# Kernel optimization log

Hardware: AMD Instinct MI355X
Metric: run time of the kernel (lower is better)

## Reference

```python
import jax, jax.numpy as jnp
import numpy as np

C = 512
NH = 4
HD = C // NH
G = 32  # min(32, C) and C % 32 == 0
EPS = 1e-5


def setup_inputs() -> dict:
    key = jax.random.key(0)
    ks = jax.random.split(key, 11)
    s = 1.0 / np.sqrt(C)
    return {
        "x": jax.random.normal(ks[0], (16, C, 32, 32), dtype=jnp.float32),
        "gamma": jnp.ones((C,), jnp.float32),
        "beta": jnp.zeros((C,), jnp.float32),
        "wq": jax.random.normal(ks[1], (C, C), jnp.float32) * s,
        "bq": jax.random.normal(ks[2], (C,), jnp.float32) * 0.01,
        "wk": jax.random.normal(ks[3], (C, C), jnp.float32) * s,
        "bk": jax.random.normal(ks[4], (C,), jnp.float32) * 0.01,
        "wv": jax.random.normal(ks[5], (C, C), jnp.float32) * s,
        "bv": jax.random.normal(ks[6], (C,), jnp.float32) * 0.01,
        "wp": jax.random.normal(ks[7], (C, C), jnp.float32) * s,
        "bp": jax.random.normal(ks[8], (C,), jnp.float32) * 0.01,
    }


def _group_norm(x, gamma, beta):
    b, c, h, w = x.shape
    xr = x.reshape(b, G, c // G, h, w)
    mean = xr.mean(axis=(2, 3, 4), keepdims=True)
    var = xr.var(axis=(2, 3, 4), keepdims=True)
    xn = ((xr - mean) * jax.lax.rsqrt(var + EPS)).reshape(b, c, h, w)
    return xn * gamma[None, :, None, None] + beta[None, :, None, None]


def _conv1x1(x, w, b):
    # 1x1 conv == per-position channel GEMM
    return jnp.einsum('oc,bchw->bohw', w, x) + b[None, :, None, None]


def reference(x, gamma, beta, wq, bq, wk, bk, wv, bv, wp, bp):
    b, c, h, w = x.shape
    hw = h * w
    scale = HD ** (-0.5)
    hn = _group_norm(x, gamma, beta)
    q = _conv1x1(hn, wq, bq).reshape(b, NH, HD, hw)
    k = _conv1x1(hn, wk, bk).reshape(b, NH, HD, hw)
    v = _conv1x1(hn, wv, bv).reshape(b, NH, HD, hw)
    attn = jnp.einsum('bhdq,bhdk->bhqk', q, k) * scale  # [b, nh, hw, hw]
    attn = jax.nn.softmax(attn, axis=-1)
    out = jnp.einsum('bhqk,bhdk->bhdq', attn, v)  # [b, nh, hd, hw]
    out = out.reshape(b, c, h, w)
    out = _conv1x1(out, wp, bp)
    return x + out
```

## Files before the change

### kernel.cpp

```cpp
#include <hip/hip_runtime.h>
#include <math.h>

#define CCH 512
#define NH 4
#define HD 128
#define HW 1024
#define BATCH 16
#define EPS 1e-5f

typedef __attribute__((ext_vector_type(8))) short bfrag;
typedef __attribute__((ext_vector_type(4))) float f4;
typedef __attribute__((ext_vector_type(16))) float f16v;

static __device__ __forceinline__ unsigned short f2bf(float f) {
  union { float f; unsigned u; } v;
  v.f = f;
  unsigned r = v.u + 0x7fff + ((v.u >> 16) & 1);
  return (unsigned short)(r >> 16);
}
static __device__ __forceinline__ unsigned cvt_pk_bf16(float a, float b) {
  unsigned r;
  asm("v_cvt_pk_bf16_f32 %0, %1, %2" : "=v"(r) : "v"(a), "v"(b));
  return r;
}
#if defined(__has_builtin) && __has_builtin(__builtin_amdgcn_exp2f)
#define EXP2(x) __builtin_amdgcn_exp2f(x)
#else
#define EXP2(x) __expf((x) * 0.6931471805599453f)
#endif
static __device__ __forceinline__ void ldg_lds16(const unsigned short* g,
                                                 unsigned short* l) {
  __builtin_amdgcn_global_load_lds(
      (const __attribute__((address_space(1))) unsigned int*)g,
      (__attribute__((address_space(3))) unsigned int*)l, 16, 0, 0);
}

#define QSCALE (0.08838834764831845f * 1.4426950408889634f)

#define SWZ(r) (((r) ^ ((r) >> 2)) & 3)

__global__ __launch_bounds__(256) void gnw_kernel(
    const float* __restrict__ x, const float* __restrict__ gamma,
    const float* __restrict__ beta, unsigned short* __restrict__ hn,
    const float* __restrict__ wq, const float* __restrict__ wk,
    const float* __restrict__ wv, const float* __restrict__ wp,
    unsigned short* __restrict__ wB) {
  int bx = blockIdx.x;
  int t = threadIdx.x;
  if (bx >= 512) {
    int i0 = bx - 512;
    int mat = i0 >> 8;
    const float* srcs[4] = {wq, wk, wv, wp};
    const float* s = srcs[mat];
    unsigned short* dp = wB + (size_t)mat * CCH * CCH;
    int i = (i0 & 255) * 256 + t;
    f4 v = ((const f4*)s)[i];
    uint2 o;
    o.x = cvt_pk_bf16(v.x, v.y);
    o.y = cvt_pk_bf16(v.z, v.w);
    *(uint2*)&((ushort4*)dp)[i] = o;
    return;
  }
  int b = bx >> 5, g = bx & 31;
  const float* xp = x + ((size_t)b * CCH + g * 16) * HW;
  float s = 0.f, ss = 0.f;
  const f4* xp4 = (const f4*)xp;
  f4 vv[16];
#pragma unroll
  for (int c = 0; c < 16; ++c) {
    f4 v = xp4[c * 256 + t];
    vv[c] = v;
    s += v.x + v.y + v.z + v.w;
    ss += v.x * v.x + v.y * v.y + v.z * v.z + v.w * v.w;
  }
#pragma unroll
  for (int off = 32; off > 0; off >>= 1) {
    s += __shfl_xor(s, off);
    ss += __shfl_xor(ss, off);
  }
  __shared__ float rs[4], rss[4];
  int w = t >> 6;
  if ((t & 63) == 0) { rs[w] = s; rss[w] = ss; }
  __syncthreads();
  s = rs[0] + rs[1] + rs[2] + rs[3];
  ss = rss[0] + rss[1] + rss[2] + rss[3];
  const float invn = 1.f / (16 * HW);
  float mean = s * invn;
  float var = ss * invn - mean * mean;
  float rstd = rsqrtf(var + EPS);
  float a_[16], b_[16];
#pragma unroll
  for (int c = 0; c < 16; ++c) {
    float gm = gamma[g * 16 + c] * rstd;
    a_[c] = gm;
    b_[c] = beta[g * 16 + c] - mean * gm;
  }
#pragma unroll
  for (int i = 0; i < 4; ++i) {
    int p = 4 * t + i;
    uint4 u0, u1;
    u0.x = cvt_pk_bf16(vv[0][i] * a_[0] + b_[0], vv[1][i] * a_[1] + b_[1]);
    u0.y = cvt_pk_bf16(vv[2][i] * a_[2] + b_[2], vv[3][i] * a_[3] + b_[3]);
    u0.z = cvt_pk_bf16(vv[4][i] * a_[4] + b_[4], vv[5][i] * a_[5] + b_[5]);
    u0.w = cvt_pk_bf16(vv[6][i] * a_[6] + b_[6], vv[7][i] * a_[7] + b_[7]);
    u1.x = cvt_pk_bf16(vv[8][i] * a_[8] + b_[8], vv[9][i] * a_[9] + b_[9]);
    u1.y = cvt_pk_bf16(vv[10][i] * a_[10] + b_[10], vv[11][i] * a_[11] + b_[11]);
    u1.z = cvt_pk_bf16(vv[12][i] * a_[12] + b_[12], vv[13][i] * a_[13] + b_[13]);
    u1.w = cvt_pk_bf16(vv[14][i] * a_[14] + b_[14], vv[15][i] * a_[15] + b_[15]);
    unsigned short* dst = hn + ((size_t)b * HW + p) * CCH + g * 16;
    *(uint4*)dst = u0;
    *(uint4*)(dst + 8) = u1;
  }
}

template <int MODE>
__global__ __launch_bounds__(256, 3) void mm_kernel(
    const unsigned short* __restrict__ Xt, const unsigned short* __restrict__ Wb,
    const float* __restrict__ b0, const float* __restrict__ b1,
    const float* __restrict__ resid,
    unsigned short* __restrict__ O0, unsigned short* __restrict__ O1,
    float* __restrict__ Ofp) {
  int b = blockIdx.z;
  int p0 = blockIdx.x * 128;
  int c0g = blockIdx.y * 128;
  __shared__ __align__(16) unsigned short S_[24576];
  int t = threadIdx.x;
  int w = t >> 6, lane = t & 63, l15 = lane & 15, quad = lane >> 4;
  int wp = (w & 1) * 64, wc = (w >> 1) * 64;
  const unsigned short* Xb = Xt + (size_t)b * HW * CCH;
  const unsigned short* Wr = Wb + (size_t)c0g * CCH;
  f4 acc[4][4] = {};
  auto stage = [&](int k0, int bi) {
    unsigned short* Xd = S_ + bi * 8192;
    unsigned short* Wd = Xd + 4096;
#pragma unroll
    for (int j = 0; j < 2; ++j) {
      int chk = w * 2 + j;
      int r = chk * 16 + (lane >> 2);
      int c = (lane & 3) ^ SWZ(r);
      ldg_lds16(&Xb[(size_t)(p0 + r) * CCH + k0 + c * 8], Xd + chk * 512);
      ldg_lds16(&Wr[(size_t)r * CCH + k0 + c * 8], Wd + chk * 512);
    }
  };
  stage(0, 0);
  stage(32, 1);
  int cur = 0;
  for (int k0 = 0; k0 < CCH; k0 += 32) {
    if (k0 < CCH - 32)
      asm volatile("s_waitcnt vmcnt(4)" ::: "memory");
    else
      asm volatile("s_waitcnt vmcnt(0)" ::: "memory");
    __builtin_amdgcn_s_barrier();
    __builtin_amdgcn_sched_barrier(0);
    if (k0 + 64 < CCH) stage(k0 + 64, cur ? cur - 1 : 2);
    const unsigned short* Xc = S_ + cur * 8192;
    const unsigned short* Wc = Xc + 4096;
    bfrag af[4], bf[4];
#pragma unroll
    for (int pt = 0; pt < 4; ++pt) {
      int r = wp + pt * 16 + l15;
      af[pt] = *(const bfrag*)&Xc[r * 32 + ((quad ^ SWZ(r)) << 3)];
    }
#pragma unroll
    for (int ct = 0; ct < 4; ++ct) {
      int r = wc + ct * 16 + l15;
      bf[ct] = *(const bfrag*)&Wc[r * 32 + ((quad ^ SWZ(r)) << 3)];
    }
#pragma unroll
    for (int pt = 0; pt < 4; ++pt)
#pragma unroll
      for (int ct = 0; ct < 4; ++ct) {
        if (MODE == 0)
          acc[pt][ct] = __builtin_amdgcn_mfma_f32_16x16x32_bf16(
              bf[ct], af[pt], acc[pt][ct], 0, 0, 0);
        else
          acc[pt][ct] = __builtin_amdgcn_mfma_f32_16x16x32_bf16(
              af[pt], bf[ct], acc[pt][ct], 0, 0, 0);
      }
    cur = cur == 2 ? 0 : cur + 1;
  }
  if (MODE == 0) {
    int mat = c0g >> 9;
    int c0 = c0g & 511;
    const float* bias = mat ? b1 : b0;
    unsigned short* O = mat ? O1 : O0;
    const float sc = mat ? 1.0f : QSCALE;
    __syncthreads();
#pragma unroll
    for (int ct = 0; ct < 4; ++ct) {
      f4 bi = *(const f4*)&bias[c0 + wc + ct * 16 + quad * 4];
      int g = (wc >> 2) + ct * 4 + quad;
#pragma unroll
      for (int pt = 0; pt < 4; ++pt) {
        int pos = wp + pt * 16 + l15;
        f4 v = acc[pt][ct];
        uint2 d;
        d.x = cvt_pk_bf16((v.x + bi.x) * sc, (v.y + bi.y) * sc);
        d.y = cvt_pk_bf16((v.z + bi.z) * sc, (v.w + bi.w) * sc);
        int gs = g ^ ((pos & 7) << 1);
        *(uint2*)&S_[pos * 128 + gs * 4] = d;
      }
    }
    __syncthreads();
    unsigned short* Op = O + (size_t)b * HW * CCH;
#pragma unroll
    for (int it = 0; it < 8; ++it) {
      int row = w * 32 + it * 4 + (lane >> 4);
      int g0 = (2 * l15) ^ ((row & 7) << 1);
      uint4 val = *(const uint4*)&S_[row * 128 + g0 * 4];
      *(uint4*)&Op[(size_t)(p0 + row) * CCH + c0 + l15 * 8] = val;
    }
  } else if (MODE == 1) {
#pragma unroll
    for (int ct = 0; ct < 4; ++ct) {
      int ch = c0g + wc + ct * 16 + l15;
      float bi = b0[ch];
      unsigned short* Op = O0 + (size_t)b * CCH * HW;
#pragma unroll
      for (int pt = 0; pt < 4; ++pt) {
        int pos = p0 + wp + pt * 16 + quad * 4;
        f4 v = acc[pt][ct];
        uint2 st;
        st.x = cvt_pk_bf16(v.x + bi, v.y + bi);
        st.y = cvt_pk_bf16(v.z + bi, v.w + bi);
        *(uint2*)&Op[(size_t)ch * HW + pos] = st;
      }
    }
  } else {
#pragma unroll
    for (int ct = 0; ct < 4; ++ct) {
      int ch = c0g + wc + ct * 16 + l15;
      float bi = b0[ch];
#pragma unroll
      for (int pt = 0; pt < 4; ++pt) {
        int pos = p0 + wp + pt * 16 + quad * 4;
        f4 v = acc[pt][ct];
        size_t off = (size_t)b * CCH * HW + (size_t)ch * HW + pos;
        float4 rv = *(const float4*)&resid[off];
        float4 st;
        st.x = v.x + bi + rv.x; st.y = v.y + bi + rv.y;
        st.z = v.z + bi + rv.z; st.w = v.w + bi + rv.w;
        *(float4*)&Ofp[off] = st;
      }
    }
  }
}

__global__ __launch_bounds__(256, 2) void attn_kernel(
    const unsigned short* __restrict__ Qt, const unsigned short* __restrict__ Kt,
    const unsigned short* __restrict__ Vc, unsigned short* __restrict__ Ot) {
  int bh = blockIdx.x;
  int b = bh >> 2, h = bh & 3;
  int q0 = blockIdx.y * 128;
  int t = threadIdx.x;
  int w = t >> 6, lane = t & 63;
  int l31 = lane & 31, half = lane >> 5;
  __shared__ __align__(16) unsigned short Ks[2][64 * 128];
  __shared__ __align__(16) unsigned short Vs[2][128 * 64];
  int q = q0 + w * 32 + l31;
  const unsigned short* Kbase = Kt + (size_t)b * HW * CCH + h * HD;
  const unsigned short* Vbase = Vc + ((size_t)b * CCH + h * HD) * HW;
  bfrag qf[8];
#pragma unroll
  for (int ks = 0; ks < 8; ++ks)
    qf[ks] = *(const bfrag*)&Qt[((size_t)b * HW + q) * CCH + h * HD +
                                ks * 16 + half * 8];
  f16v o[4] = {};
  float ls[4] = {};
  auto stage = [&](int kt, int bi) {
    int kk0 = kt * 64;
#pragma unroll
    for (int j = 0; j < 4; ++j) {
      int chk = w * 4 + j;
      {
        int r = chk * 4 + (lane >> 4);
        int c = (lane & 15) ^ (r & 15);
        ldg_lds16(&Kbase[(size_t)(kk0 + r) * CCH + c * 8], &Ks[bi][chk * 512]);
      }
      {
        int r = chk * 8 + (lane >> 3);
        int c = (lane & 7) ^ (r & 7);
        ldg_lds16(&Vbase[(size_t)r * HW + kk0 + c * 8], &Vs[bi][chk * 512]);
      }
    }
  };
  stage(0, 0);
  for (int kt = 0; kt < 16; ++kt) {
    __syncthreads();
    if (kt < 15) stage(kt + 1, (kt + 1) & 1);
    const unsigned short* K_ = Ks[kt & 1];
    const unsigned short* V_ = Vs[kt & 1];
    f16v S[2] = {};
    __builtin_amdgcn_s_setprio(1);
#pragma unroll
    for (int ks = 0; ks < 8; ++ks) {
      int c16 = ks * 2 + half;
#pragma unroll
      for (int mt = 0; mt < 2; ++mt) {
        int r = mt * 32 + l31;
        bfrag kf = *(const bfrag*)&K_[r * 128 + ((c16 ^ (r & 15)) << 3)];
        S[mt] = __builtin_amdgcn_mfma_f32_32x32x16_bf16(kf, qf[ks], S[mt],
                                                        0, 0, 0);
      }
    }
    __builtin_amdgcn_s_setprio(0);
    unsigned pd[16];
#pragma unroll
    for (int mt = 0; mt < 2; ++mt)
#pragma unroll
      for (int i = 0; i < 8; ++i) {
        float p0 = EXP2(S[mt][2 * i]);
        float p1 = EXP2(S[mt][2 * i + 1]);
        ls[i & 3] += p0 + p1;
        pd[mt * 8 + i] = cvt_pk_bf16(p0, p1);
      }
#pragma unroll
    for (int mt = 0; mt < 2; ++mt)
#pragma unroll
      for (int s = 0; s < 2; ++s) {
        int base = mt * 8 + s * 4;
        unsigned a0 = pd[base + 0], a1 = pd[base + 1];
        unsigned c0 = pd[base + 2], c1 = pd[base + 3];
        asm("v_permlane32_swap_b32 %0, %1" : "+v"(a0), "+v"(c0));
        asm("v_permlane32_swap_b32 %0, %1" : "+v"(a1), "+v"(c1));
        union { unsigned u[4]; bfrag f; } pf;
        pf.u[0] = a0; pf.u[1] = a1; pf.u[2] = c0; pf.u[3] = c1;
        int c8 = (mt * 2 + s) * 2 + half;
        __builtin_amdgcn_s_setprio(1);
#pragma unroll
        for (int dt = 0; dt < 4; ++dt) {
          int r = dt * 32 + l31;
          bfrag vf = *(const bfrag*)&V_[r * 64 + ((c8 ^ (r & 7)) << 3)];
          o[dt] = __builtin_amdgcn_mfma_f32_32x32x16_bf16(vf, pf.f, o[dt],
                                                          0, 0, 0);
        }
        __builtin_amdgcn_s_setprio(0);
      }
  }
  float lrow = (ls[0] + ls[1]) + (ls[2] + ls[3]);
  lrow += __shfl_xor(lrow, 32);
  float inv = 1.f / lrow;
  unsigned short* Op = Ot + ((size_t)b * HW + q) * CCH + h * HD;
#pragma unroll
  for (int dt = 0; dt < 4; ++dt)
#pragma unroll
    for (int rg = 0; rg < 4; ++rg) {
      int d = dt * 32 + rg * 8 + half * 4;
      uint2 st;
      st.x = cvt_pk_bf16(o[dt][rg * 4 + 0] * inv, o[dt][rg * 4 + 1] * inv);
      st.y = cvt_pk_bf16(o[dt][rg * 4 + 2] * inv, o[dt][rg * 4 + 3] * inv);
      *(uint2*)&Op[d] = st;
    }
}

extern "C" void kernel_launch(void* const* d_in, const int* in_sizes, int n_in,
                              void* d_out, int out_size, void* d_ws,
                              size_t ws_size, hipStream_t stream) {
  const float* x = (const float*)d_in[0];
  const float* gamma = (const float*)d_in[1];
  const float* beta = (const float*)d_in[2];
  const float* wq = (const float*)d_in[3];
  const float* bq = (const float*)d_in[4];
  const float* wk = (const float*)d_in[5];
  const float* bk = (const float*)d_in[6];
  const float* wv = (const float*)d_in[7];
  const float* bv = (const float*)d_in[8];
  const float* wp = (const float*)d_in[9];
  const float* bp = (const float*)d_in[10];

  const size_t TS = (size_t)BATCH * HW * CCH;
  unsigned short* wB = (unsigned short*)d_ws;
  unsigned short* hn = wB + (size_t)4 * CCH * CCH;
  unsigned short* Qt = hn + TS;
  unsigned short* Kt = Qt + TS;
  unsigned short* Vc = Kt + TS;
  unsigned short* Ot = hn;

  gnw_kernel<<<dim3(1536), 256, 0, stream>>>(x, gamma, beta, hn,
                                             wq, wk, wv, wp, wB);
  mm_kernel<0><<<dim3(8, 8, BATCH), 256, 0, stream>>>(
      hn, wB, bq, bk, nullptr, Qt, Kt, nullptr);
  mm_kernel<1><<<dim3(8, 4, BATCH), 256, 0, stream>>>(
      hn, wB + (size_t)2 * CCH * CCH, bv, nullptr, nullptr, Vc, nullptr,
      nullptr);
  attn_kernel<<<dim3(64, 8), 256, 0, stream>>>(Qt, Kt, Vc, Ot);
  mm_kernel<2><<<dim3(8, 4, BATCH), 256, 0, stream>>>(
      Ot, wB + (size_t)3 * CCH * CCH, bp, nullptr, x, nullptr, nullptr,
      (float*)d_out);
}
```

Measured before the change: 207.2 us.

## Add dedicated 256x256-tile QK projection kernel with ping-pong scheduled MFMA

Replaces the 128x128 mm_kernel<0> path for the Q/K projections with a new 512-thread kernel that computes 256x256 output tiles. It uses double-buffered direct global-to-LDS loads, splits prefetch into four chunks interleaved with MFMA phases, and raises priority with s_setprio around the MFMA blocks. The aim is more operand reuse per LDS load and better overlap of loads with math. In exchange it needs 128 KB of LDS per block and launches only 256 blocks, so occupancy and load balance may suffer.

```diff
diff --git a/kernel.cpp b/kernel.cpp
--- a/kernel.cpp
+++ b/kernel.cpp
@@ -113,13 +113,175 @@
   }
 }
 
+__global__ __launch_bounds__(512, 2) void qk_kernel(
+    const unsigned short* __restrict__ Xt, const unsigned short* __restrict__ Wb,
+    const float* __restrict__ bq, const float* __restrict__ bk,
+    unsigned short* __restrict__ Qt, unsigned short* __restrict__ Kt) {
+  int b = blockIdx.z;
+  int p0 = blockIdx.x * 256;
+  int c0g = blockIdx.y * 256;
+  __shared__ __align__(16) unsigned short S_[65536];
+  int t = threadIdx.x;
+  int w = t >> 6, lane = t & 63, l15 = lane & 15, quad = lane >> 4;
+  int wp = (w & 1) * 128;
+  int wc = (w >> 1) * 64;
+  const unsigned short* Xb = Xt + (size_t)b * HW * CCH;
+  const unsigned short* Wr = Wb + (size_t)c0g * CCH;
+  f4 acc[8][4] = {};
+  auto stageA = [&](int k0, int bi, int j) {
+    int chk = w * 4 + j;
+    int r = chk * 8 + (lane >> 3);
+    int c = (lane & 7) ^ (r & 7);
+    ldg_lds16(&Xb[(size_t)(p0 + r) * CCH + k0 + c * 8],
+              S_ + bi * 32768 + chk * 512);
+  };
+  auto stageB = [&](int k0, int bi, int j) {
+    int chk = w * 4 + j;
+    int r = chk * 8 + (lane >> 3);
+    int c = (lane & 7) ^ (r & 7);
+    ldg_lds16(&Wr[(size_t)r * CCH + k0 + c * 8],
+              S_ + bi * 32768 + 16384 + chk * 512);
+  };
+#pragma unroll
+  for (int j = 0; j < 4; ++j) { stageA(0, 0, j); stageB(0, 0, j); }
+  __syncthreads();
+  for (int kt = 0; kt < 8; ++kt) {
+    int cur = kt & 1;
+    const unsigned short* A_ = S_ + cur * 32768;
+    const unsigned short* B_ = A_ + 16384;
+    int k0n = kt * 64 + 64;
+    bool pre = kt < 7;
+    bfrag af0[8], af1[8], bf[4];
+    if (pre) { stageA(k0n, cur ^ 1, 0); stageB(k0n, cur ^ 1, 0); }
+#pragma unroll
+    for (int pt = 0; pt < 4; ++pt)
+#pragma unroll
+      for (int ks = 0; ks < 2; ++ks) {
+        int r = wp + pt * 16 + l15;
+        af0[pt * 2 + ks] =
+            *(const bfrag*)&A_[r * 64 + (((ks * 4 + quad) ^ (r & 7)) << 3)];
+      }
+#pragma unroll
+    for (int ct = 0; ct < 2; ++ct)
+#pragma unroll
+      for (int ks = 0; ks < 2; ++ks) {
+        int r = wc + ct * 16 + l15;
+        bf[ct * 2 + ks] =
+            *(const bfrag*)&B_[r * 64 + (((ks * 4 + quad) ^ (r & 7)) << 3)];
+      }
+    __builtin_amdgcn_s_barrier();
+    __builtin_amdgcn_s_setprio(1);
+#pragma unroll
+    for (int pt = 0; pt < 4; ++pt)
+#pragma unroll
+      for (int ct = 0; ct < 2; ++ct)
+#pragma unroll
+        for (int ks = 0; ks < 2; ++ks)
+          acc[pt][ct] = __builtin_amdgcn_mfma_f32_16x16x32_bf16(
+              bf[ct * 2 + ks], af0[pt * 2 + ks], acc[pt][ct], 0, 0, 0);
+    __builtin_amdgcn_s_setprio(0);
+    if (pre) { stageA(k0n, cur ^ 1, 1); stageB(k0n, cur ^ 1, 1); }
+#pragma unroll
+    for (int pt = 0; pt < 4; ++pt)
+#pragma unroll
+      for (int ks = 0; ks < 2; ++ks) {
+        int r = wp + 64 + pt * 16 + l15;
+        af1[pt * 2 + ks] =
+            *(const bfrag*)&A_[r * 64 + (((ks * 4 + quad) ^ (r & 7)) << 3)];
+      }
+    __builtin_amdgcn_s_barrier();
+    __builtin_amdgcn_s_setprio(1);
+#pragma unroll
+    for (int pt = 0; pt < 4; ++pt)
+#pragma unroll
+      for (int ct = 0; ct < 2; ++ct)
+#pragma unroll
+        for (int ks = 0; ks < 2; ++ks)
+          acc[pt + 4][ct] = __builtin_amdgcn_mfma_f32_16x16x32_bf16(
+              bf[ct * 2 + ks], af1[pt * 2 + ks], acc[pt + 4][ct], 0, 0, 0);
+    __builtin_amdgcn_s_setprio(0);
+    if (pre) { stageA(k0n, cur ^ 1, 2); stageB(k0n, cur ^ 1, 2); }
+#pragma unroll
+    for (int ct = 0; ct < 2; ++ct)
+#pragma unroll
+      for (int ks = 0; ks < 2; ++ks) {
+        int r = wc + (ct + 2) * 16 + l15;
+        bf[ct * 2 + ks] =
+            *(const bfrag*)&B_[r * 64 + (((ks * 4 + quad) ^ (r & 7)) << 3)];
+      }
+    __builtin_amdgcn_s_barrier();
+    __builtin_amdgcn_s_setprio(1);
+#pragma unroll
+    for (int pt = 0; pt < 4; ++pt)
+#pragma unroll
+      for (int ct = 0; ct < 2; ++ct)
+#pragma unroll
+        for (int ks = 0; ks < 2; ++ks)
+          acc[pt + 4][ct + 2] = __builtin_amdgcn_mfma_f32_16x16x32_bf16(
+              bf[ct * 2 + ks], af1[pt * 2 + ks], acc[pt + 4][ct + 2], 0, 0, 0);
+    __builtin_amdgcn_s_setprio(0);
+    if (pre) { stageA(k0n, cur ^ 1, 3); stageB(k0n, cur ^ 1, 3); }
+    __builtin_amdgcn_s_barrier();
+    __builtin_amdgcn_s_setprio(1);
+#pragma unroll
+    for (int pt = 0; pt < 4; ++pt)
+#pragma unroll
+      for (int ct = 0; ct < 2; ++ct)
+#pragma unroll
+        for (int ks = 0; ks < 2; ++ks)
+          acc[pt][ct + 2] = __builtin_amdgcn_mfma_f32_16x16x32_bf16(
+              bf[ct * 2 + ks], af0[pt * 2 + ks], acc[pt][ct + 2], 0, 0, 0);
+    __builtin_amdgcn_s_setprio(0);
+    if (pre) {
+      asm volatile("s_waitcnt vmcnt(0)" ::: "memory");
+      __builtin_amdgcn_s_barrier();
+    }
+  }
+  __syncthreads();
+  int mat = c0g >> 9;
+  int c0 = c0g & 511;
+  const float* bias = mat ? bk : bq;
+  unsigned short* O = mat ? Kt : Qt;
+  const float sc = mat ? 1.0f : QSCALE;
+  unsigned short* Op = O + (size_t)b * HW * CCH;
+  int wcl = wc & 127;
+  int myhalf = wc >> 7;
+#pragma unroll
+  for (int h = 0; h < 2; ++h) {
+    if (myhalf == h) {
+#pragma unroll
+      for (int ct = 0; ct < 4; ++ct) {
+        f4 bi = *(const f4*)&bias[c0 + h * 128 + wcl + ct * 16 + quad * 4];
+        int g = (wcl >> 2) + ct * 4 + quad;
+#pragma unroll
+        for (int pt = 0; pt < 8; ++pt) {
+          int pos = wp + pt * 16 + l15;
+          f4 v = acc[pt][ct];
+          uint2 d;
+          d.x = cvt_pk_bf16((v.x + bi.x) * sc, (v.y + bi.y) * sc);
+          d.y = cvt_pk_bf16((v.z + bi.z) * sc, (v.w + bi.w) * sc);
+          int gs = g ^ ((pos & 7) << 1);
+          *(uint2*)&S_[pos * 128 + gs * 4] = d;
+        }
+      }
+    }
+    __syncthreads();
+#pragma unroll
+    for (int it = 0; it < 8; ++it) {
+      int row = w * 32 + it * 4 + (lane >> 4);
+      int g0 = (2 * l15) ^ ((row & 7) << 1);
+      uint4 val = *(const uint4*)&S_[row * 128 + g0 * 4];
+      *(uint4*)&Op[(size_t)(p0 + row) * CCH + c0 + h * 128 + l15 * 8] = val;
+    }
+    if (h == 0) __syncthreads();
+  }
+}
+
 template <int MODE>
 __global__ __launch_bounds__(256, 3) void mm_kernel(
     const unsigned short* __restrict__ Xt, const unsigned short* __restrict__ Wb,
-    const float* __restrict__ b0, const float* __restrict__ b1,
-    const float* __restrict__ resid,
-    unsigned short* __restrict__ O0, unsigned short* __restrict__ O1,
-    float* __restrict__ Ofp) {
+    const float* __restrict__ b0, const float* __restrict__ resid,
+    unsigned short* __restrict__ O0, float* __restrict__ Ofp) {
   int b = blockIdx.z;
   int p0 = blockIdx.x * 128;
   int c0g = blockIdx.y * 128;
@@ -169,48 +331,12 @@
 #pragma unroll
     for (int pt = 0; pt < 4; ++pt)
 #pragma unroll
-      for (int ct = 0; ct < 4; ++ct) {
-        if (MODE == 0)
-          acc[pt][ct] = __builtin_amdgcn_mfma_f32_16x16x32_bf16(
-              bf[ct], af[pt], acc[pt][ct], 0, 0, 0);
-        else
-          acc[pt][ct] = __builtin_amdgcn_mfma_f32_16x16x32_bf16(
-              af[pt], bf[ct], acc[pt][ct], 0, 0, 0);
-      }
+      for (int ct = 0; ct < 4; ++ct)
+        acc[pt][ct] = __builtin_amdgcn_mfma_f32_16x16x32_bf16(
+            af[pt], bf[ct], acc[pt][ct], 0, 0, 0);
     cur = cur == 2 ? 0 : cur + 1;
   }
-  if (MODE == 0) {
-    int mat = c0g >> 9;
-    int c0 = c0g & 511;
-    const float* bias = mat ? b1 : b0;
-    unsigned short* O = mat ? O1 : O0;
-    const float sc = mat ? 1.0f : QSCALE;
-    __syncthreads();
-#pragma unroll
-    for (int ct = 0; ct < 4; ++ct) {
-      f4 bi = *(const f4*)&bias[c0 + wc + ct * 16 + quad * 4];
-      int g = (wc >> 2) + ct * 4 + quad;
-#pragma unroll
-      for (int pt = 0; pt < 4; ++pt) {
-        int pos = wp + pt * 16 + l15;
-        f4 v = acc[pt][ct];
-        uint2 d;
-        d.x = cvt_pk_bf16((v.x + bi.x) * sc, (v.y + bi.y) * sc);
-        d.y = cvt_pk_bf16((v.z + bi.z) * sc, (v.w + bi.w) * sc);
-        int gs = g ^ ((pos & 7) << 1);
-        *(uint2*)&S_[pos * 128 + gs * 4] = d;
-      }
-    }
-    __syncthreads();
-    unsigned short* Op = O + (size_t)b * HW * CCH;
-#pragma unroll
-    for (int it = 0; it < 8; ++it) {
-      int row = w * 32 + it * 4 + (lane >> 4);
-      int g0 = (2 * l15) ^ ((row & 7) << 1);
-      uint4 val = *(const uint4*)&S_[row * 128 + g0 * 4];
-      *(uint4*)&Op[(size_t)(p0 + row) * CCH + c0 + l15 * 8] = val;
-    }
-  } else if (MODE == 1) {
+  if (MODE == 1) {
 #pragma unroll
     for (int ct = 0; ct < 4; ++ct) {
       int ch = c0g + wc + ct * 16 + l15;
@@ -378,13 +504,10 @@
 
   gnw_kernel<<<dim3(1536), 256, 0, stream>>>(x, gamma, beta, hn,
                                              wq, wk, wv, wp, wB);
-  mm_kernel<0><<<dim3(8, 8, BATCH), 256, 0, stream>>>(
-      hn, wB, bq, bk, nullptr, Qt, Kt, nullptr);
+  qk_kernel<<<dim3(4, 4, BATCH), 512, 0, stream>>>(hn, wB, bq, bk, Qt, Kt);
   mm_kernel<1><<<dim3(8, 4, BATCH), 256, 0, stream>>>(
-      hn, wB + (size_t)2 * CCH * CCH, bv, nullptr, nullptr, Vc, nullptr,
-      nullptr);
+      hn, wB + (size_t)2 * CCH * CCH, bv, nullptr, Vc, nullptr);
   attn_kernel<<<dim3(64, 8), 256, 0, stream>>>(Qt, Kt, Vc, Ot);
   mm_kernel<2><<<dim3(8, 4, BATCH), 256, 0, stream>>>(
-      Ot, wB + (size_t)3 * CCH * CCH, bp, nullptr, x, nullptr, nullptr,
-      (float*)d_out);
-}
+      Ot, wB + (size_t)3 * CCH * CCH, bp, x, nullptr, (float*)d_out);
+}
```

New measurement: 205.8 us. About the same (-0.7%).
